# Optimization experiments

Hardware: AMD Instinct MI355X
Metric: run time of the kernel (lower is better)

The kernel has to match this reference:

```python
import jax, jax.numpy as jnp
import numpy as np

B, N, D, H = 2, 2048, 1024, 16
HS = D // H  # head size = 64


def setup_inputs() -> dict:
    key = jax.random.key(0)
    k1, k2, k3 = jax.random.split(key, 3)
    x = jax.random.normal(k1, (B, N, D), dtype=jnp.float32)
    attn_mask = jnp.ones((B, N), dtype=jnp.float32)  # all tokens valid
    # qkv projection: Dense(d*3, use_bias=False)
    Wqkv = jax.random.normal(k2, (D, 3 * D), dtype=jnp.float32) * (D ** -0.5)
    # out projection: Dense(d) with default bias
    Wout = jax.random.normal(k3, (D, D), dtype=jnp.float32) * (D ** -0.5)
    bout = jnp.zeros((D,), dtype=jnp.float32)
    return {"x": x, "attn_mask": attn_mask, "Wqkv": Wqkv, "Wout": Wout, "bout": bout}


def reference(x, attn_mask, Wqkv, Wout, bout):
    b, n, d = x.shape
    h, hs = H, d // H
    qkv = x @ Wqkv  # (b, n, 3d)
    q, k, v = jnp.split(qkv, 3, axis=-1)
    # (b, n, d) -> (b, h, n, hs)
    q = q.reshape(b, n, h, hs).transpose(0, 2, 1, 3)
    k = k.reshape(b, n, h, hs).transpose(0, 2, 1, 3)
    v = v.reshape(b, n, h, hs).transpose(0, 2, 1, 3)
    # NOTE: module scales by full d**-0.5, not head_size**-0.5 (faithful)
    scores = jnp.einsum('bhqe,bhke->bhqk', q, k) * (d ** -0.5)  # (b,h,n,n)
    # multiplicative padding mask: (b,1,n,1)*(b,1,1,n)
    m = attn_mask[:, None, :, None] * attn_mask[:, None, None, :]
    scores = scores * m
    scores = jnp.where(scores == 0.0, -jnp.inf, scores)
    weights = jax.nn.softmax(scores, axis=-1)
    ctx = jnp.einsum('bhqk,bhke->bhqe', weights, v)  # (b,h,n,hs)
    ctx = ctx.transpose(0, 2, 1, 3).reshape(b, n, d)
    return ctx @ Wout + bout
```

## Files before the change

kernel.cpp:

```cpp
#include <hip/hip_runtime.h>

typedef __attribute__((ext_vector_type(8))) short short8;
typedef __attribute__((ext_vector_type(4))) short s16x4;
typedef __attribute__((ext_vector_type(8))) __bf16 bf16x8;
typedef __attribute__((ext_vector_type(4))) __bf16 bf16x4;
typedef __attribute__((ext_vector_type(2))) __bf16 bf16x2;
typedef __attribute__((ext_vector_type(4))) float f32x4;
typedef __attribute__((ext_vector_type(2))) float f32x2;
typedef __attribute__((ext_vector_type(4))) unsigned uint4v;
typedef __attribute__((ext_vector_type(2))) unsigned uint2v;

__device__ inline f32x4 mfma_bf16(short8 a, short8 b, f32x4 c) {
    return __builtin_amdgcn_mfma_f32_16x16x32_bf16(
        __builtin_bit_cast(bf16x8, a), __builtin_bit_cast(bf16x8, b), c, 0, 0, 0);
}
__device__ inline f32x4 mfma16(uint2v a, uint2v b, f32x4 c) {
#if __has_builtin(__builtin_amdgcn_mfma_f32_16x16x16_bf16)
    return __builtin_amdgcn_mfma_f32_16x16x16_bf16(
        __builtin_bit_cast(bf16x4, a), __builtin_bit_cast(bf16x4, b), c, 0, 0, 0);
#else
    return __builtin_amdgcn_mfma_f32_16x16x16bf16_1k(
        __builtin_bit_cast(s16x4, a), __builtin_bit_cast(s16x4, b), c, 0, 0, 0);
#endif
}

__device__ inline float fexp2(float x) {
#if __has_builtin(__builtin_amdgcn_exp2f)
    return __builtin_amdgcn_exp2f(x);
#else
    return exp2f(x);
#endif
}

__device__ inline short f2b(float f) {
    __bf16 h = (__bf16)f;
    return __builtin_bit_cast(short, h);
}
__device__ inline unsigned pkbf(float a, float b) {
    f32x2 v; v[0] = a; v[1] = b;
    bf16x2 h = __builtin_convertvector(v, bf16x2);
    return __builtin_bit_cast(unsigned, h);
}

__device__ inline short8 ld8(const short* p) { return *(const short8*)p; }
__device__ inline short8 ld8(const float* p) {
    f32x4 a = *(const f32x4*)p;
    f32x4 b = *(const f32x4*)(p + 4);
    uint4v q;
    q[0] = pkbf(a[0], a[1]); q[1] = pkbf(a[2], a[3]);
    q[2] = pkbf(b[0], b[1]); q[3] = pkbf(b[2], b[3]);
    return __builtin_bit_cast(short8, q);
}
__device__ inline void storeC(short* C, size_t i, float v) { C[i] = f2b(v); }
__device__ inline void storeC(float* C, size_t i, float v) { C[i] = v; }

__device__ inline void gload16(const short* g, short* l) {
    __builtin_amdgcn_global_load_lds(
        (const __attribute__((address_space(1))) unsigned*)g,
        (__attribute__((address_space(3))) unsigned*)l, 16, 0, 0);
}

#define QSCALE 0.04508422052265167f

__global__ __launch_bounds__(256) void prep(
    const float* __restrict__ x, short* __restrict__ xb,
    const float* __restrict__ Wqkv, short* __restrict__ wqkvt,
    const float* __restrict__ Wout, short* __restrict__ woutt)
{
    const int bid = blockIdx.x;
    const int tid = threadIdx.x;
    if (bid < 2048) {
        size_t i = ((size_t)bid * 256 + tid) * 8;
        *(short8*)(xb + i) = ld8(x + i);
        return;
    }
    __shared__ short T[64 * 72];
    const float* W; short* Wt; int K, N, n0, k0;
    if (bid < 2816) {
        const int b2 = bid - 2048;
        W = Wqkv; Wt = wqkvt; K = 1024; N = 3072;
        n0 = (b2 % 48) * 64; k0 = (b2 / 48) * 64;
    } else {
        const int b3 = bid - 2816;
        W = Wout; Wt = woutt; K = 1024; N = 1024;
        n0 = (b3 & 15) * 64; k0 = (b3 >> 4) * 64;
    }
    {
        const int kl = tid >> 2, nc = (tid & 3) * 16;
        const float* src = W + (size_t)(k0 + kl) * N + n0 + nc;
        float v[16];
        *(f32x4*)&v[0]  = *(const f32x4*)(src + 0);
        *(f32x4*)&v[4]  = *(const f32x4*)(src + 4);
        *(f32x4*)&v[8]  = *(const f32x4*)(src + 8);
        *(f32x4*)&v[12] = *(const f32x4*)(src + 12);
        #pragma unroll
        for (int j = 0; j < 16; ++j) T[(nc + j) * 72 + kl] = f2b(v[j]);
    }
    __syncthreads();
    {
        const int nl = tid >> 2, kc = (tid & 3) * 16;
        short8 w0 = *(const short8*)&T[nl * 72 + kc];
        short8 w1 = *(const short8*)&T[nl * 72 + kc + 8];
        short* dst = Wt + (size_t)(n0 + nl) * K + k0 + kc;
        *(short8*)dst = w0;
        *(short8*)(dst + 8) = w1;
    }
}

__global__ __launch_bounds__(256) void vtrans(
    const short* __restrict__ qkv, short* __restrict__ vt)
{
    __shared__ short T[64 * 72];
    const int tid = threadIdx.x;
    const int nt = blockIdx.x * 64, bh = blockIdx.y;
    const int b = bh >> 4, h = bh & 15;
    {
        const int tok = tid >> 2, dc = (tid & 3) * 16;
        const short* src = qkv + ((size_t)b * 2048 + nt + tok) * 3072 + 2048 + h * 64 + dc;
        short8 v0 = *(const short8*)src;
        short8 v1 = *(const short8*)(src + 8);
        #pragma unroll
        for (int j = 0; j < 8; ++j) {
            T[(dc + j) * 72 + tok]     = v0[j];
            T[(dc + 8 + j) * 72 + tok] = v1[j];
        }
    }
    __syncthreads();
    {
        const int dim = tid >> 2, kc = (tid & 3) * 16;
        short8 w0 = *(const short8*)&T[dim * 72 + kc];
        short8 w1 = *(const short8*)&T[dim * 72 + kc + 8];
        short* dst = vt + ((size_t)bh * 64 + dim) * 2048 + nt + kc;
        *(short8*)dst = w0;
        *(short8*)(dst + 8) = w1;
    }
}

template <bool QSC, bool ADD_BIAS, typename TC>
__global__ __launch_bounds__(256, 4) void gemm128(
    const short* __restrict__ A, const short* __restrict__ Bt,
    const float* __restrict__ bias, TC* __restrict__ C,
    int M, int N, int K, int lda)
{
    __shared__ short A_s0[128 * 32];
    __shared__ short A_s1[128 * 32];
    __shared__ short B_s0[128 * 32];
    __shared__ short B_s1[128 * 32];
    const int tid  = threadIdx.x;
    const int lane = tid & 63;
    const int wave = tid >> 6;
    const int quad = lane >> 4;
    const int l16  = lane & 15;
    const int wr   = wave >> 1;
    const int wc   = wave & 1;
    const int bm   = blockIdx.y * 128;
    const int bn   = blockIdx.x * 128;

    f32x4 acc[4][4];
    #pragma unroll
    for (int i = 0; i < 4; ++i)
        #pragma unroll
        for (int j = 0; j < 4; ++j)
            acc[i][j] = f32x4{0.f, 0.f, 0.f, 0.f};

    const int srow = tid >> 2;
    const int schk = tid & 3;
    const int sg   = (schk ^ ((srow >> 1) & 3)) * 8;
    const short* ap0 = A  + (size_t)(bm + srow) * lda + sg;
    const short* ap1 = A  + (size_t)(bm + 64 + srow) * lda + sg;
    const short* bp0 = Bt + (size_t)(bn + srow) * K   + sg;
    const short* bp1 = Bt + (size_t)(bn + 64 + srow) * K   + sg;
    const int lofs0 = wave * 512;
    const int lofs1 = 2048 + wave * 512;

    const int xr = (quad ^ ((l16 >> 1) & 3)) * 8;

#define STAGE_G(As, Bs, koff)                  \
    gload16(ap0 + (koff), (As) + lofs0);       \
    gload16(ap1 + (koff), (As) + lofs1);       \
    gload16(bp0 + (koff), (Bs) + lofs0);       \
    gload16(bp1 + (koff), (Bs) + lofs1);

#define COMPUTE_G(As, Bs)                                                   \
    {                                                                       \
        short8 a[4], b[4];                                                  \
        _Pragma("unroll")                                                   \
        for (int i = 0; i < 4; ++i)                                         \
            a[i] = *(const short8*)&(As)[(wr * 64 + i * 16 + l16) * 32 + xr]; \
        _Pragma("unroll")                                                   \
        for (int j = 0; j < 4; ++j)                                         \
            b[j] = *(const short8*)&(Bs)[(wc * 64 + j * 16 + l16) * 32 + xr]; \
        _Pragma("unroll")                                                   \
        for (int i = 0; i < 4; ++i)                                         \
            _Pragma("unroll")                                               \
            for (int j = 0; j < 4; ++j)                                     \
                acc[i][j] = mfma_bf16(a[i], b[j], acc[i][j]);               \
    }

    STAGE_G(A_s0, B_s0, 0);
    __syncthreads();

    for (int k0 = 0; k0 < K; k0 += 64) {
        if (k0 + 32 < K) { STAGE_G(A_s1, B_s1, k0 + 32); }
        COMPUTE_G(A_s0, B_s0);
        __syncthreads();
        if (k0 + 64 < K) { STAGE_G(A_s0, B_s0, k0 + 64); }
        COMPUTE_G(A_s1, B_s1);
        __syncthreads();
    }
#undef STAGE_G
#undef COMPUTE_G

    const float scale = (QSC && bn < 1024) ? QSCALE : 1.0f;
    #pragma unroll
    for (int i = 0; i < 4; ++i) {
        #pragma unroll
        for (int j = 0; j < 4; ++j) {
            #pragma unroll
            for (int r = 0; r < 4; ++r) {
                int row = bm + wr * 64 + i * 16 + quad * 4 + r;
                int col = bn + wc * 64 + j * 16 + l16;
                float v = acc[i][j][r] * scale;
                if (ADD_BIAS) v += bias[col];
                storeC(C, (size_t)row * N + col, v);
            }
        }
    }
}

template <bool ADD_BIAS, typename TC>
__global__ __launch_bounds__(256, 4) void gemm64(
    const short* __restrict__ A, const short* __restrict__ Bt,
    const float* __restrict__ bias, TC* __restrict__ C,
    int M, int N, int K, int lda)
{
    __shared__ short A_s0[64 * 32];
    __shared__ short A_s1[64 * 32];
    __shared__ short B_s0[128 * 32];
    __shared__ short B_s1[128 * 32];
    const int tid  = threadIdx.x;
    const int lane = tid & 63;
    const int wave = tid >> 6;
    const int quad = lane >> 4;
    const int l16  = lane & 15;
    const int wr   = wave >> 1;
    const int wc   = wave & 1;
    const int bm   = blockIdx.y * 64;
    const int bn   = blockIdx.x * 128;

    f32x4 acc[2][4];
    #pragma unroll
    for (int i = 0; i < 2; ++i)
        #pragma unroll
        for (int j = 0; j < 4; ++j)
            acc[i][j] = f32x4{0.f, 0.f, 0.f, 0.f};

    const int srow = tid >> 2;
    const int schk = tid & 3;
    const int sg   = (schk ^ ((srow >> 1) & 3)) * 8;
    const short* ap0 = A  + (size_t)(bm + srow) * lda + sg;
    const short* bp0 = Bt + (size_t)(bn + srow) * K   + sg;
    const short* bp1 = Bt + (size_t)(bn + 64 + srow) * K + sg;
    const int lofs0 = wave * 512;
    const int lofs1 = 2048 + wave * 512;

    const int xr = (quad ^ ((l16 >> 1) & 3)) * 8;

#define STAGE_H(As, Bs, koff)                  \
    gload16(ap0 + (koff), (As) + lofs0);       \
    gload16(bp0 + (koff), (Bs) + lofs0);       \
    gload16(bp1 + (koff), (Bs) + lofs1);

#define COMPUTE_H(As, Bs)                                                   \
    {                                                                       \
        short8 a[2], b[4];                                                  \
        _Pragma("unroll")                                                   \
        for (int i = 0; i < 2; ++i)                                         \
            a[i] = *(const short8*)&(As)[(wr * 32 + i * 16 + l16) * 32 + xr]; \
        _Pragma("unroll")                                                   \
        for (int j = 0; j < 4; ++j)                                         \
            b[j] = *(const short8*)&(Bs)[(wc * 64 + j * 16 + l16) * 32 + xr]; \
        _Pragma("unroll")                                                   \
        for (int i = 0; i < 2; ++i)                                         \
            _Pragma("unroll")                                               \
            for (int j = 0; j < 4; ++j)                                     \
                acc[i][j] = mfma_bf16(a[i], b[j], acc[i][j]);               \
    }

    STAGE_H(A_s0, B_s0, 0);
    __syncthreads();

    for (int k0 = 0; k0 < K; k0 += 64) {
        if (k0 + 32 < K) { STAGE_H(A_s1, B_s1, k0 + 32); }
        COMPUTE_H(A_s0, B_s0);
        __syncthreads();
        if (k0 + 64 < K) { STAGE_H(A_s0, B_s0, k0 + 64); }
        COMPUTE_H(A_s1, B_s1);
        __syncthreads();
    }
#undef STAGE_H
#undef COMPUTE_H

    #pragma unroll
    for (int i = 0; i < 2; ++i) {
        #pragma unroll
        for (int j = 0; j < 4; ++j) {
            #pragma unroll
            for (int r = 0; r < 4; ++r) {
                int row = bm + wr * 32 + i * 16 + quad * 4 + r;
                int col = bn + wc * 64 + j * 16 + l16;
                float v = acc[i][j][r];
                if (ADD_BIAS) v += bias[col];
                storeC(C, (size_t)row * N + col, v);
            }
        }
    }
}

__global__ __launch_bounds__(256) void attn128(
    short* __restrict__ qkv, const short* __restrict__ vt)
{
    __shared__ short Ks[128 * 72];
    __shared__ short Vs[16 * 520];

    const int tid  = threadIdx.x;
    const int lane = tid & 63;
    const int wave = tid >> 6;
    const int quad = lane >> 4;
    const int l16  = lane & 15;
    const int bh   = blockIdx.y, b = bh >> 4, h = bh & 15;
    const int qb   = blockIdx.x * 128;
    const size_t rowbase = (size_t)b * 2048;

    short8 aq[2][2];
    #pragma unroll
    for (int qg = 0; qg < 2; ++qg) {
        const short* qp = qkv + (rowbase + qb + wave * 32 + qg * 16 + l16) * 3072 + h * 64;
        aq[qg][0] = *(const short8*)(qp + quad * 8);
        aq[qg][1] = *(const short8*)(qp + 32 + quad * 8);
    }

    f32x4 o[2][4];
    #pragma unroll
    for (int qg = 0; qg < 2; ++qg)
        #pragma unroll
        for (int c = 0; c < 4; ++c) o[qg][c] = f32x4{0.f, 0.f, 0.f, 0.f};
    float rsum[2] = {0.f, 0.f};

    const int kkey = tid >> 1, kdc = (tid & 1) * 32;
    const int vdim = tid >> 2, vg0 = (tid & 3) * 4;
    const short* kbase = qkv + (rowbase + kkey) * 3072 + 1024 + h * 64 + kdc;
    const short* vbase = vt + ((size_t)bh * 64 + vdim) * 2048 + vg0 * 8;

    short8 kr0 = *(const short8*)(kbase);
    short8 kr1 = *(const short8*)(kbase + 8);
    short8 kr2 = *(const short8*)(kbase + 16);
    short8 kr3 = *(const short8*)(kbase + 24);
    short8 vr0 = *(const short8*)(vbase);
    short8 vr1 = *(const short8*)(vbase + 8);
    short8 vr2 = *(const short8*)(vbase + 16);
    short8 vr3 = *(const short8*)(vbase + 24);

    for (int kt = 0; kt < 2048; kt += 128) {
        __syncthreads();
        *(short8*)&Ks[kkey * 72 + kdc]      = kr0;
        *(short8*)&Ks[kkey * 72 + kdc + 8]  = kr1;
        *(short8*)&Ks[kkey * 72 + kdc + 16] = kr2;
        *(short8*)&Ks[kkey * 72 + kdc + 24] = kr3;
        *(short8*)&Vs[(vg0 + 0) * 520 + vdim * 8] = vr0;
        *(short8*)&Vs[(vg0 + 1) * 520 + vdim * 8] = vr1;
        *(short8*)&Vs[(vg0 + 2) * 520 + vdim * 8] = vr2;
        *(short8*)&Vs[(vg0 + 3) * 520 + vdim * 8] = vr3;
        if (kt + 128 < 2048) {
            const short* kp = kbase + (size_t)(kt + 128) * 3072;
            kr0 = *(const short8*)(kp);
            kr1 = *(const short8*)(kp + 8);
            kr2 = *(const short8*)(kp + 16);
            kr3 = *(const short8*)(kp + 24);
            const short* vp = vbase + kt + 128;
            vr0 = *(const short8*)(vp);
            vr1 = *(const short8*)(vp + 8);
            vr2 = *(const short8*)(vp + 16);
            vr3 = *(const short8*)(vp + 24);
        }
        __syncthreads();

        #pragma unroll
        for (int cc = 0; cc < 2; ++cc) {
            f32x4 st[2][4];
            #pragma unroll
            for (int c4 = 0; c4 < 4; ++c4) {
                const int c = cc * 4 + c4;
                short8 ka0 = *(const short8*)&Ks[(c * 16 + l16) * 72 + quad * 8];
                short8 ka1 = *(const short8*)&Ks[(c * 16 + l16) * 72 + 32 + quad * 8];
                #pragma unroll
                for (int qg = 0; qg < 2; ++qg) {
                    f32x4 z = f32x4{0.f, 0.f, 0.f, 0.f};
                    z = mfma_bf16(ka0, aq[qg][0], z);
                    st[qg][c4] = mfma_bf16(ka1, aq[qg][1], z);
                }
            }
            uint2v pa[2][4];
            #pragma unroll
            for (int qg = 0; qg < 2; ++qg) {
                #pragma unroll
                for (int c4 = 0; c4 < 4; ++c4) {
                    float p0 = fexp2(st[qg][c4][0]);
                    float p1 = fexp2(st[qg][c4][1]);
                    float p2 = fexp2(st[qg][c4][2]);
                    float p3 = fexp2(st[qg][c4][3]);
                    rsum[qg] += (p0 + p1) + (p2 + p3);
                    uint2v pk;
                    pk[0] = pkbf(p0, p1);
                    pk[1] = pkbf(p2, p3);
                    pa[qg][c4] = pk;
                }
            }
            #pragma unroll
            for (int c2 = 0; c2 < 4; ++c2) {
                #pragma unroll
                for (int c4 = 0; c4 < 4; ++c4) {
                    const int c = cc * 4 + c4;
                    uint2v bv = *(const uint2v*)&Vs[(2 * c + (quad >> 1)) * 520
                                                    + (c2 * 16 + l16) * 8
                                                    + (quad & 1) * 4];
                    #pragma unroll
                    for (int qg = 0; qg < 2; ++qg)
                        o[qg][c2] = mfma16(pa[qg][c4], bv, o[qg][c2]);
                }
            }
        }
    }

    #pragma unroll
    for (int qg = 0; qg < 2; ++qg) {
        rsum[qg] += __shfl_xor(rsum[qg], 16, 64);
        rsum[qg] += __shfl_xor(rsum[qg], 32, 64);
    }

    #pragma unroll
    for (int qg = 0; qg < 2; ++qg) {
        #pragma unroll
        for (int r = 0; r < 4; ++r) {
            float inv = 1.0f / __shfl(rsum[qg], quad * 4 + r, 64);
            size_t row = rowbase + qb + wave * 32 + qg * 16 + quad * 4 + r;
            #pragma unroll
            for (int c2 = 0; c2 < 4; ++c2)
                qkv[row * 3072 + h * 64 + c2 * 16 + l16] = f2b(o[qg][c2][r] * inv);
        }
    }
}

extern "C" void kernel_launch(void* const* d_in, const int* in_sizes, int n_in,
                              void* d_out, int out_size, void* d_ws, size_t ws_size,
                              hipStream_t stream)
{
    const float* x    = (const float*)d_in[0];
    const float* Wqkv = (const float*)d_in[2];
    const float* Wout = (const float*)d_in[3];
    const float* bout = (const float*)d_in[4];
    float* out = (float*)d_out;

    short* qkv   = (short*)d_ws;
    short* wqkvt = qkv + (size_t)4096 * 3072;
    short* woutt = wqkvt + (size_t)3072 * 1024;
    short* xbf   = (short*)d_out;
    short* vtbuf = xbf + (size_t)4096 * 1024;

    dim3 blk(256);
    prep<<<dim3(3072), blk, 0, stream>>>(x, xbf, Wqkv, wqkvt, Wout, woutt);
    gemm128<true, false, short><<<dim3(24, 32), blk, 0, stream>>>(
        xbf, wqkvt, nullptr, qkv, 4096, 3072, 1024, 1024);
    vtrans<<<dim3(32, 32), blk, 0, stream>>>(qkv, vtbuf);
    attn128<<<dim3(16, 32), blk, 0, stream>>>(qkv, vtbuf);
    gemm64<true, float><<<dim3(8, 64), blk, 0, stream>>>(
        qkv, woutt, bout, out, 4096, 1024, 1024, 3072);
}
```

Baseline: 190.5 us.

## Split key tiles across two wave groups in attention and reduce via LDS

Doubles the attention block to 512 threads: four query waves are duplicated into two key-halves, each processing half of every 128-key tile, with global-to-LDS loads spread over more threads. Partial outputs and row sums from the second group are reduced through shared memory before normalization and store. Aims to raise wave occupancy and latency hiding per CU, at the cost of an extra LDS reduction and more register pressure under the 512-thread launch bound.

```diff
diff --git a/kernel.cpp b/kernel.cpp
--- a/kernel.cpp
+++ b/kernel.cpp
@@ -317,15 +317,18 @@
     }
 }
 
-__global__ __launch_bounds__(256) void attn128(
+__global__ __launch_bounds__(512, 4) void attn128(
     short* __restrict__ qkv, const short* __restrict__ vt)
 {
-    __shared__ short Ks[128 * 72];
-    __shared__ short Vs[16 * 520];
+    __shared__ short SM[128 * 72 + 16 * 520];
+    short* Ks = SM;
+    short* Vs = SM + 128 * 72;
 
     const int tid  = threadIdx.x;
     const int lane = tid & 63;
     const int wave = tid >> 6;
+    const int qw   = wave & 3;
+    const int kw   = wave >> 2;
     const int quad = lane >> 4;
     const int l16  = lane & 15;
     const int bh   = blockIdx.y, b = bh >> 4, h = bh & 15;
@@ -335,7 +338,7 @@
     short8 aq[2][2];
     #pragma unroll
     for (int qg = 0; qg < 2; ++qg) {
-        const short* qp = qkv + (rowbase + qb + wave * 32 + qg * 16 + l16) * 3072 + h * 64;
+        const short* qp = qkv + (rowbase + qb + qw * 32 + qg * 16 + l16) * 3072 + h * 64;
         aq[qg][0] = *(const short8*)(qp + quad * 8);
         aq[qg][1] = *(const short8*)(qp + 32 + quad * 8);
     }
@@ -347,46 +350,34 @@
         for (int c = 0; c < 4; ++c) o[qg][c] = f32x4{0.f, 0.f, 0.f, 0.f};
     float rsum[2] = {0.f, 0.f};
 
-    const int kkey = tid >> 1, kdc = (tid & 1) * 32;
-    const int vdim = tid >> 2, vg0 = (tid & 3) * 4;
+    const int kkey = tid >> 2, kdc = (tid & 3) * 16;
+    const int vdim = tid >> 3, vg0 = (tid & 7) * 2;
     const short* kbase = qkv + (rowbase + kkey) * 3072 + 1024 + h * 64 + kdc;
     const short* vbase = vt + ((size_t)bh * 64 + vdim) * 2048 + vg0 * 8;
 
     short8 kr0 = *(const short8*)(kbase);
     short8 kr1 = *(const short8*)(kbase + 8);
-    short8 kr2 = *(const short8*)(kbase + 16);
-    short8 kr3 = *(const short8*)(kbase + 24);
     short8 vr0 = *(const short8*)(vbase);
     short8 vr1 = *(const short8*)(vbase + 8);
-    short8 vr2 = *(const short8*)(vbase + 16);
-    short8 vr3 = *(const short8*)(vbase + 24);
 
     for (int kt = 0; kt < 2048; kt += 128) {
         __syncthreads();
-        *(short8*)&Ks[kkey * 72 + kdc]      = kr0;
-        *(short8*)&Ks[kkey * 72 + kdc + 8]  = kr1;
-        *(short8*)&Ks[kkey * 72 + kdc + 16] = kr2;
-        *(short8*)&Ks[kkey * 72 + kdc + 24] = kr3;
+        *(short8*)&Ks[kkey * 72 + kdc]     = kr0;
+        *(short8*)&Ks[kkey * 72 + kdc + 8] = kr1;
         *(short8*)&Vs[(vg0 + 0) * 520 + vdim * 8] = vr0;
         *(short8*)&Vs[(vg0 + 1) * 520 + vdim * 8] = vr1;
-        *(short8*)&Vs[(vg0 + 2) * 520 + vdim * 8] = vr2;
-        *(short8*)&Vs[(vg0 + 3) * 520 + vdim * 8] = vr3;
         if (kt + 128 < 2048) {
             const short* kp = kbase + (size_t)(kt + 128) * 3072;
             kr0 = *(const short8*)(kp);
             kr1 = *(const short8*)(kp + 8);
-            kr2 = *(const short8*)(kp + 16);
-            kr3 = *(const short8*)(kp + 24);
             const short* vp = vbase + kt + 128;
             vr0 = *(const short8*)(vp);
             vr1 = *(const short8*)(vp + 8);
-            vr2 = *(const short8*)(vp + 16);
-            vr3 = *(const short8*)(vp + 24);
-        }
-        __syncthreads();
-
-        #pragma unroll
-        for (int cc = 0; cc < 2; ++cc) {
+        }
+        __syncthreads();
+
+        const int cc = kw;
+        {
             f32x4 st[2][4];
             #pragma unroll
             for (int c4 = 0; c4 < 4; ++c4) {
@@ -432,6 +423,35 @@
         }
     }
 
+    __syncthreads();
+    float* xo = (float*)SM;
+    float* xr2 = xo + 4 * 64 * 32;
+    if (kw == 1) {
+        float* xp = xo + (qw * 64 + lane) * 32;
+        #pragma unroll
+        for (int qg = 0; qg < 2; ++qg)
+            #pragma unroll
+            for (int c2 = 0; c2 < 4; ++c2)
+                *(f32x4*)(xp + qg * 16 + c2 * 4) = o[qg][c2];
+        float* rp = xr2 + (qw * 64 + lane) * 2;
+        rp[0] = rsum[0]; rp[1] = rsum[1];
+    }
+    __syncthreads();
+    if (kw == 1) return;
+
+    {
+        const float* xp = xo + (qw * 64 + lane) * 32;
+        #pragma unroll
+        for (int qg = 0; qg < 2; ++qg)
+            #pragma unroll
+            for (int c2 = 0; c2 < 4; ++c2) {
+                f32x4 t = *(const f32x4*)(xp + qg * 16 + c2 * 4);
+                o[qg][c2] += t;
+            }
+        const float* rp = xr2 + (qw * 64 + lane) * 2;
+        rsum[0] += rp[0]; rsum[1] += rp[1];
+    }
+
     #pragma unroll
     for (int qg = 0; qg < 2; ++qg) {
         rsum[qg] += __shfl_xor(rsum[qg], 16, 64);
@@ -443,7 +463,7 @@
         #pragma unroll
         for (int r = 0; r < 4; ++r) {
             float inv = 1.0f / __shfl(rsum[qg], quad * 4 + r, 64);
-            size_t row = rowbase + qb + wave * 32 + qg * 16 + quad * 4 + r;
+            size_t row = rowbase + qb + qw * 32 + qg * 16 + quad * 4 + r;
             #pragma unroll
             for (int c2 = 0; c2 < 4; ++c2)
                 qkv[row * 3072 + h * 64 + c2 * 16 + l16] = f2b(o[qg][c2][r] * inv);
@@ -472,7 +492,7 @@
     gemm128<true, false, short><<<dim3(24, 32), blk, 0, stream>>>(
         xbf, wqkvt, nullptr, qkv, 4096, 3072, 1024, 1024);
     vtrans<<<dim3(32, 32), blk, 0, stream>>>(qkv, vtbuf);
-    attn128<<<dim3(16, 32), blk, 0, stream>>>(qkv, vtbuf);
+    attn128<<<dim3(16, 32), dim3(512), 0, stream>>>(qkv, vtbuf);
     gemm64<true, float><<<dim3(8, 64), blk, 0, stream>>>(
         qkv, woutt, bout, out, 4096, 1024, 1024, 3072);
 }
```

Result: slower. 222.8 us (+17.0%).

## Double-buffer attention K/V LDS tiles and swizzle GEMM workgroup order

Applied to the files above, without the earlier changes.

The attention kernel now keeps two LDS buffers for K and V tiles. It writes the next tile into the spare buffer while computing on the current one, which removes one barrier per iteration and overlaps staging with MFMA work. Both GEMM kernels remap workgroup IDs so that consecutive launched blocks are spread across strided tile positions, likely to balance XCD/L2 locality. The cost is double the LDS in attention, which may lower occupancy, and the remap assumes the grid size divides by 8.

```diff
diff --git a/kernel.cpp b/kernel.cpp
--- a/kernel.cpp
+++ b/kernel.cpp
@@ -153,8 +153,11 @@
     const int l16  = lane & 15;
     const int wr   = wave >> 1;
     const int wc   = wave & 1;
-    const int bm   = blockIdx.y * 128;
-    const int bn   = blockIdx.x * 128;
+    const int nwg = gridDim.x * gridDim.y;
+    const int lid = blockIdx.y * gridDim.x + blockIdx.x;
+    const int sid = (lid & 7) * (nwg >> 3) + (lid >> 3);
+    const int bm  = (sid / gridDim.x) * 128;
+    const int bn  = (sid % gridDim.x) * 128;
 
     f32x4 acc[4][4];
     #pragma unroll
@@ -245,8 +248,11 @@
     const int l16  = lane & 15;
     const int wr   = wave >> 1;
     const int wc   = wave & 1;
-    const int bm   = blockIdx.y * 64;
-    const int bn   = blockIdx.x * 128;
+    const int nwg = gridDim.x * gridDim.y;
+    const int lid = blockIdx.y * gridDim.x + blockIdx.x;
+    const int sid = (lid & 7) * (nwg >> 3) + (lid >> 3);
+    const int bm  = (sid / gridDim.x) * 64;
+    const int bn  = (sid % gridDim.x) * 128;
 
     f32x4 acc[2][4];
     #pragma unroll
@@ -320,8 +326,10 @@
 __global__ __launch_bounds__(256) void attn128(
     short* __restrict__ qkv, const short* __restrict__ vt)
 {
-    __shared__ short Ks[128 * 72];
-    __shared__ short Vs[16 * 520];
+    __shared__ short Ks0[128 * 72];
+    __shared__ short Vs0[16 * 520];
+    __shared__ short Ks1[128 * 72];
+    __shared__ short Vs1[16 * 520];
 
     const int tid  = threadIdx.x;
     const int lane = tid & 63;
@@ -352,17 +360,21 @@
     const short* kbase = qkv + (rowbase + kkey) * 3072 + 1024 + h * 64 + kdc;
     const short* vbase = vt + ((size_t)bh * 64 + vdim) * 2048 + vg0 * 8;
 
-    short8 kr0 = *(const short8*)(kbase);
-    short8 kr1 = *(const short8*)(kbase + 8);
-    short8 kr2 = *(const short8*)(kbase + 16);
-    short8 kr3 = *(const short8*)(kbase + 24);
-    short8 vr0 = *(const short8*)(vbase);
-    short8 vr1 = *(const short8*)(vbase + 8);
-    short8 vr2 = *(const short8*)(vbase + 16);
-    short8 vr3 = *(const short8*)(vbase + 24);
-
-    for (int kt = 0; kt < 2048; kt += 128) {
-        __syncthreads();
+    short8 kr0, kr1, kr2, kr3, vr0, vr1, vr2, vr3;
+
+    auto prefetch = [&](int kt) {
+        const short* kp = kbase + (size_t)kt * 3072;
+        kr0 = *(const short8*)(kp);
+        kr1 = *(const short8*)(kp + 8);
+        kr2 = *(const short8*)(kp + 16);
+        kr3 = *(const short8*)(kp + 24);
+        const short* vp = vbase + kt;
+        vr0 = *(const short8*)(vp);
+        vr1 = *(const short8*)(vp + 8);
+        vr2 = *(const short8*)(vp + 16);
+        vr3 = *(const short8*)(vp + 24);
+    };
+    auto stage = [&](short* Ks, short* Vs) {
         *(short8*)&Ks[kkey * 72 + kdc]      = kr0;
         *(short8*)&Ks[kkey * 72 + kdc + 8]  = kr1;
         *(short8*)&Ks[kkey * 72 + kdc + 16] = kr2;
@@ -371,20 +383,8 @@
         *(short8*)&Vs[(vg0 + 1) * 520 + vdim * 8] = vr1;
         *(short8*)&Vs[(vg0 + 2) * 520 + vdim * 8] = vr2;
         *(short8*)&Vs[(vg0 + 3) * 520 + vdim * 8] = vr3;
-        if (kt + 128 < 2048) {
-            const short* kp = kbase + (size_t)(kt + 128) * 3072;
-            kr0 = *(const short8*)(kp);
-            kr1 = *(const short8*)(kp + 8);
-            kr2 = *(const short8*)(kp + 16);
-            kr3 = *(const short8*)(kp + 24);
-            const short* vp = vbase + kt + 128;
-            vr0 = *(const short8*)(vp);
-            vr1 = *(const short8*)(vp + 8);
-            vr2 = *(const short8*)(vp + 16);
-            vr3 = *(const short8*)(vp + 24);
-        }
-        __syncthreads();
-
+    };
+    auto compute = [&](const short* Ks, const short* Vs) {
         #pragma unroll
         for (int cc = 0; cc < 2; ++cc) {
             f32x4 st[2][4];
@@ -430,6 +430,22 @@
                 }
             }
         }
+    };
+
+    prefetch(0);
+    stage(Ks0, Vs0);
+    prefetch(128);
+    __syncthreads();
+
+    for (int t = 0; t < 16; t += 2) {
+        stage(Ks1, Vs1);
+        if (t + 2 < 16) prefetch((t + 2) * 128);
+        compute(Ks0, Vs0);
+        __syncthreads();
+        if (t + 2 < 16) stage(Ks0, Vs0);
+        if (t + 3 < 16) prefetch((t + 3) * 128);
+        compute(Ks1, Vs1);
+        __syncthreads();
     }
 
     #pragma unroll
```

Measured after the change: 197.5 us. 1.04x slower.
